# Optimization experiments

Hardware: AMD Instinct MI355X
Metric: run time of the kernel (lower is better)

## Reference

```python
import jax, jax.numpy as jnp
import numpy as np

TEMP = 0.07
EPS = 1e-6
NORM_EPS = 1e-12  # F.normalize default eps
LN_EPS = 1e-5

B, D, H, W = 32, 256, 64, 64
K = 256
DFF = 2048


def _l2norm(v, axis):
    n = jnp.sqrt(jnp.sum(v * v, axis=axis, keepdims=True))
    return v / jnp.maximum(n, NORM_EPS)


def _layernorm(v, g, b):
    mu = jnp.mean(v, axis=-1, keepdims=True)
    var = jnp.mean((v - mu) ** 2, axis=-1, keepdims=True)
    return (v - mu) * jax.lax.rsqrt(var + LN_EPS) * g + b


def setup_inputs() -> dict:
    key = jax.random.key(0)
    ks = jax.random.split(key, 8)
    s1 = 1.0 / np.sqrt(D)
    s2 = 1.0 / np.sqrt(DFF)
    return {
        "x": jax.random.normal(ks[0], (B, D, H, W), jnp.float32),
        "tgt": jax.random.normal(ks[1], (B, K, D), jnp.float32),
        "w1": jax.random.uniform(ks[2], (DFF, D), jnp.float32, -s1, s1),
        "b1": jax.random.uniform(ks[3], (DFF,), jnp.float32, -s1, s1),
        "w2": jax.random.uniform(ks[4], (D, DFF), jnp.float32, -s2, s2),
        "b2": jax.random.uniform(ks[5], (D,), jnp.float32, -s2, s2),
        "g2": jnp.ones((D,), jnp.float32),
        "be2": jnp.zeros((D,), jnp.float32),
        "g3": jnp.ones((D,), jnp.float32),
        "be3": jnp.zeros((D,), jnp.float32),
    }


def reference(x, tgt, w1, b1, w2, b2, g2, be2, g3, be3):
    # slot cross-attention with L2-normalized q/k
    tn = _l2norm(tgt, axis=2)           # (b,k,d)
    xn = _l2norm(x, axis=1)             # (b,d,h,w)
    dots = jnp.einsum('bkd,bdhw->bkhw', tn, xn)
    attn = jax.nn.softmax(dots / TEMP, axis=1) + EPS          # softmax over slots
    attn = attn / jnp.sum(attn, axis=(2, 3), keepdims=True)   # spatial normalization
    tgt2 = jnp.einsum('bdhw,bkhw->bkd', x, attn)
    t = _layernorm(tgt + tgt2, g2, be2)
    # FFN (dropout = identity in eval)
    ff = jnp.maximum(t @ w1.T + b1, 0.0) @ w2.T + b2
    return _layernorm(t + ff, g3, be3)
```

## Files before the change

kernel.cpp:

```cpp
#include <hip/hip_runtime.h>
#include <hip/hip_bf16.h>

using bf16 = __hip_bfloat16;

typedef __attribute__((ext_vector_type(8))) short short8;
typedef __attribute__((ext_vector_type(4))) float f32x4;

constexpr int Bb = 32, Dd = 256, HWw = 4096, Kk = 256, Ff = 2048;
constexpr float TEMP_INV = 1.0f / 0.07f;
constexpr float EPSf = 1e-6f;
constexpr float NORM_EPSf = 1e-12f;
constexpr float LN_EPSf = 1e-5f;

static __device__ __forceinline__ float b2f(bf16 v) { return __bfloat162float(v); }
static __device__ __forceinline__ bf16 f2b(float v) { return __float2bfloat16(v); }


__global__ __launch_bounds__(64) void k_tn(const float* __restrict__ tgt,
                                           bf16* __restrict__ tnbf) {
  int row = blockIdx.x;
  int b = row >> 8, slot = row & 255;
  int lane = threadIdx.x;
  const float* src = tgt + (size_t)row * Dd + lane * 4;
  float v[4];
#pragma unroll
  for (int u = 0; u < 4; u++) v[u] = src[u];
  float ss = v[0] * v[0] + v[1] * v[1] + v[2] * v[2] + v[3] * v[3];
#pragma unroll
  for (int m = 32; m >= 1; m >>= 1) ss += __shfl_xor(ss, m, 64);
  float inv = 1.0f / fmaxf(sqrtf(ss), NORM_EPSf);
  bf16 o[4] __attribute__((aligned(8)));
#pragma unroll
  for (int u = 0; u < 4; u++) o[u] = f2b(v[u] * inv);
  int s = lane >> 3;
  int q2 = (lane >> 1) & 3;
  int jh = (lane & 1) * 4;
  size_t fi = (size_t)((slot >> 4) * 64 + q2 * 16 + (slot & 15));
  *(float2*)(tnbf + ((size_t)(b * 8 + s) * 1024 + fi) * 8 + jh) = *(float2*)o;
}

__global__ __launch_bounds__(64) void k_prew1(const float* __restrict__ w1,
                                              bf16* __restrict__ w1bf) {
  int f = blockIdx.x;
  int lane = threadIdx.x;
  const float* src = w1 + (size_t)f * Dd + lane * 4;
  bf16 o[4] __attribute__((aligned(8)));
#pragma unroll
  for (int u = 0; u < 4; u++) o[u] = f2b(src[u]);
  int s = lane >> 3;
  int q2 = (lane >> 1) & 3;
  int jh = (lane & 1) * 4;
  size_t fi = (size_t)(((f & 63) >> 4) * 64 + q2 * 16 + (f & 15));
  *(float2*)(w1bf + ((size_t)((f >> 6) * 8 + s) * 256 + fi) * 8 + jh) = *(float2*)o;
}

__global__ __launch_bounds__(64) void k_prew2(const float* __restrict__ w2,
                                              bf16* __restrict__ w2bf) {
  int d = blockIdx.x;
  int lane = threadIdx.x;
  const float* src = w2 + (size_t)d * Ff + lane * 32;
  size_t gbase = (size_t)((d >> 6) * 64 + lane) * 256;
  int fbase = ((d & 63) >> 4) * 64 + (d & 15);
#pragma unroll
  for (int q2 = 0; q2 < 4; q2++) {
    float4 v0 = *(const float4*)(src + q2 * 8);
    float4 v1 = *(const float4*)(src + q2 * 8 + 4);
    bf16 o[8] __attribute__((aligned(16)));
    o[0] = f2b(v0.x); o[1] = f2b(v0.y); o[2] = f2b(v0.z); o[3] = f2b(v0.w);
    o[4] = f2b(v1.x); o[5] = f2b(v1.y); o[6] = f2b(v1.z); o[7] = f2b(v1.w);
    *(float4*)(w2bf + (gbase + fbase + q2 * 16) * 8) = *(float4*)o;
  }
}

#define MFMA16(a, b, c) __builtin_amdgcn_mfma_f32_16x16x32_bf16(a, b, c, 0, 0, 0)

__global__ __launch_bounds__(256) void k_dots(const bf16* __restrict__ tnbf,
                                              const float* __restrict__ x,
                                              bf16* __restrict__ xb_bf,
                                              bf16* __restrict__ attn_bf,
                                              float* __restrict__ S) {
  __shared__ __align__(16) char smem[39936];
  bf16* Bs8 = (bf16*)smem;
  float* ssred = (float*)(smem + 33280);
  float* nxl = (float*)(smem + 37632);
  float* red = (float*)(smem + 37888);
  int b = blockIdx.x >> 6;
  int hw0 = (blockIdx.x & 63) * 64;
  int tid = threadIdx.x;
  int wave = tid >> 6, lane = tid & 63;
  int quad = lane >> 4, nl = lane & 15;

  int dp = tid >> 4;
  int ch = tid & 15;
  int qb = dp >> 2;
  int jb = (dp & 3) * 2;

  f32x4 acc[4][4];
#pragma unroll
  for (int i = 0; i < 4; i++)
#pragma unroll
    for (int j = 0; j < 4; j++) acc[i][j] = (f32x4){0.f, 0.f, 0.f, 0.f};
  float ssp[4] = {0.f, 0.f, 0.f, 0.f};

  int spx = (hw0 >> 5) + (ch >> 3);
  int q2x = (ch >> 1) & 3;
  int jx = (ch & 1) * 4;

#pragma unroll 1
  for (int c = 0; c < 2; c++) {
    float4 va4[4], vb4[4];
#pragma unroll
    for (int q = 0; q < 4; q++) {
      const float* xr = x + (size_t)((b << 8) + (c * 4 + q) * 32 + 2 * dp) * HWw + hw0 + ch * 4;
      va4[q] = *(const float4*)xr;
      vb4[q] = *(const float4*)(xr + HWw);
    }
#pragma unroll
    for (int q = 0; q < 4; q++) {
      int s = c * 4 + q;
      float vva[4] = {va4[q].x, va4[q].y, va4[q].z, va4[q].w};
      float vvb[4] = {vb4[q].x, vb4[q].y, vb4[q].z, vb4[q].w};
      bf16 pa[4] __attribute__((aligned(8)));
      bf16 pb[4] __attribute__((aligned(8)));
#pragma unroll
      for (int jj = 0; jj < 4; jj++) {
        ssp[jj] += vva[jj] * vva[jj] + vvb[jj] * vvb[jj];
        pa[jj] = f2b(vva[jj]);
        pb[jj] = f2b(vvb[jj]);
      }
      int d0r = s * 32 + 2 * dp;
      int fiA = (d0r >> 4) * 64 + q2x * 16 + (d0r & 15);
      size_t base = ((size_t)(b * 128) + spx) * 1024;
      *(float2*)(xb_bf + (base + fiA) * 8 + jx) = *(float2*)pa;
      *(float2*)(xb_bf + (base + fiA + 1) * 8 + jx) = *(float2*)pb;
#pragma unroll
      for (int jj = 0; jj < 4; jj++) {
        int hwl = ch * 4 + jj;
        int nt = hwl >> 4;
        int li = (qb << 4) | (hwl & 15);
        union { bf16 h[2]; unsigned int u; } pk;
        pk.h[0] = pa[jj];
        pk.h[1] = pb[jj];
        *(unsigned int*)&Bs8[s * 2080 + nt * 520 + li * 8 + jb] = pk.u;
      }
    }
  }
  __syncthreads();

  short8 afp[4];
  {
    const bf16* ts0 = tnbf + (size_t)(b * 8) * 1024 * 8;
#pragma unroll
    for (int mt = 0; mt < 4; mt++)
      afp[mt] = *(const short8*)(ts0 + (size_t)(((wave << 2) + mt) * 64 + lane) * 8);
  }
  for (int s = 0; s < 8; s++) {
    short8 af[4];
#pragma unroll
    for (int mt = 0; mt < 4; mt++) af[mt] = afp[mt];
    if (s < 7) {
      const bf16* tsrc = tnbf + (size_t)(b * 8 + s + 1) * 1024 * 8;
#pragma unroll
      for (int mt = 0; mt < 4; mt++)
        afp[mt] = *(const short8*)(tsrc + (size_t)(((wave << 2) + mt) * 64 + lane) * 8);
    }
    short8 bfv[4];
#pragma unroll
    for (int nt = 0; nt < 4; nt++)
      bfv[nt] = *(const short8*)(Bs8 + s * 2080 + nt * 520 + lane * 8);
#pragma unroll
    for (int mt = 0; mt < 4; mt++)
#pragma unroll
      for (int nt = 0; nt < 4; nt++) acc[mt][nt] = MFMA16(af[mt], bfv[nt], acc[mt][nt]);
  }

#pragma unroll
  for (int jj = 0; jj < 4; jj++) ssred[(ch * 4 + jj) * 17 + dp] = ssp[jj];
  __syncthreads();
  if (tid < 64) {
    float sum = 0.f;
#pragma unroll
    for (int i = 0; i < 16; i++) sum += ssred[tid * 17 + i];
    nxl[tid] = TEMP_INV / fmaxf(sqrtf(sum), NORM_EPSf);
  }
  __syncthreads();

  float sc[4];
#pragma unroll
  for (int nt = 0; nt < 4; nt++) sc[nt] = nxl[nt * 16 + nl];
#pragma unroll
  for (int mt = 0; mt < 4; mt++)
#pragma unroll
    for (int nt = 0; nt < 4; nt++)
#pragma unroll
      for (int r = 0; r < 4; r++) acc[mt][nt][r] *= sc[nt];

  float* red2 = red + 256;

  float pmax[4];
#pragma unroll
  for (int nt = 0; nt < 4; nt++) {
    float m = acc[0][nt][0];
#pragma unroll
    for (int mt = 0; mt < 4; mt++)
#pragma unroll
      for (int r = 0; r < 4; r++) m = fmaxf(m, acc[mt][nt][r]);
    m = fmaxf(m, __shfl_xor(m, 16, 64));
    m = fmaxf(m, __shfl_xor(m, 32, 64));
    pmax[nt] = m;
  }
  if (lane < 16) {
#pragma unroll
    for (int nt = 0; nt < 4; nt++) red[((wave << 2) + nt) * 16 + nl] = pmax[nt];
  }
  __syncthreads();
  float cmax[4];
#pragma unroll
  for (int nt = 0; nt < 4; nt++) {
    float m = red[nt * 16 + nl];
#pragma unroll
    for (int w2 = 1; w2 < 4; w2++) m = fmaxf(m, red[((w2 << 2) + nt) * 16 + nl]);
    cmax[nt] = m;
  }

  float psum[4];
#pragma unroll
  for (int nt = 0; nt < 4; nt++) {
    float s = 0.f;
#pragma unroll
    for (int mt = 0; mt < 4; mt++)
#pragma unroll
      for (int r = 0; r < 4; r++) {
        float e = __expf(acc[mt][nt][r] - cmax[nt]);
        acc[mt][nt][r] = e;
        s += e;
      }
    s += __shfl_xor(s, 16, 64);
    s += __shfl_xor(s, 32, 64);
    psum[nt] = s;
  }
  if (lane < 16) {
#pragma unroll
    for (int nt = 0; nt < 4; nt++) red2[((wave << 2) + nt) * 16 + nl] = psum[nt];
  }
  __syncthreads();
  float ci[4];
#pragma unroll
  for (int nt = 0; nt < 4; nt++) {
    float s = 0.f;
#pragma unroll
    for (int w2 = 0; w2 < 4; w2++) s += red2[((w2 << 2) + nt) * 16 + nl];
    ci[nt] = 1.0f / s;
  }

#pragma unroll
  for (int mt = 0; mt < 4; mt++) {
    int slotg = (b << 8) + (wave << 6) + (mt << 4) + (quad << 2);
#pragma unroll
    for (int r = 0; r < 4; r++) {
      float rs = 0.f;
#pragma unroll
      for (int nt = 0; nt < 4; nt++) {
        bf16 hb = f2b(acc[mt][nt][r] * ci[nt] + EPSf);
        float q = b2f(hb);
        acc[mt][nt][r] = q;
        rs += q;
      }
      rs += __shfl_xor(rs, 1, 64);
      rs += __shfl_xor(rs, 2, 64);
      rs += __shfl_xor(rs, 4, 64);
      rs += __shfl_xor(rs, 8, 64);
      if (nl == 0) atomicAdd(&S[slotg + r], rs);
    }
  }

  __syncthreads();
  bf16* rp = (bf16*)smem;
  int jat = nl & 7;
#pragma unroll
  for (int h = 0; h < 2; h++) {
#pragma unroll
    for (int mt = 0; mt < 4; mt++) {
      int fi0 = ((wave << 2) + mt) * 64 + (quad << 2);
#pragma unroll
      for (int ntl = 0; ntl < 2; ntl++) {
        int nt = (h << 1) + ntl;
        int q2p = (ntl << 1) + (nl >> 3);
#pragma unroll
        for (int r = 0; r < 4; r++) {
          int fi = fi0 + q2p * 16 + r;
          int fisw = fi ^ ((fi >> 3) & 3);
          rp[fisw * 8 + jat] = f2b(acc[mt][nt][r]);
        }
      }
    }
    __syncthreads();
    size_t gbase = ((size_t)(b * 128) + (hw0 >> 5) + h) * 1024 * 8;
#pragma unroll
    for (int u = 0; u < 4; u++) {
      int fl = u * 256 + tid;
      int fg = fl ^ ((fl >> 3) & 3);
      short8 vv = *(const short8*)(rp + (size_t)fl * 8);
      *(short8*)(attn_bf + gbase + (size_t)fg * 8) = vv;
    }
    if (h == 0) __syncthreads();
  }
}

__global__ __launch_bounds__(256) void k_gemm2(const bf16* __restrict__ attn_bf,
                                               const bf16* __restrict__ xb_bf,
                                               float* __restrict__ t2) {
  int n = blockIdx.x;
  int b = n & 31;
  int r2 = n >> 5;
  int kp = r2 & 3;
  int dgrp = r2 >> 2;
  int tid = threadIdx.x;
  int wave = tid >> 6, lane = tid & 63;
  int wr = wave >> 1, wc = wave & 1;

  f32x4 acc[2][2];
#pragma unroll
  for (int i = 0; i < 2; i++)
#pragma unroll
    for (int j = 0; j < 2; j++) acc[i][j] = (f32x4){0.f, 0.f, 0.f, 0.f};

  const bf16* Abase = attn_bf + ((size_t)(b * 128) * 1024 + (size_t)(kp * 4 + wr * 2) * 64) * 8;
  const bf16* Bbase = xb_bf + ((size_t)(b * 128) * 1024 + (size_t)(dgrp * 4 + wc * 2) * 64) * 8;
#pragma unroll 4
  for (int st = 0; st < 128; st++) {
    const bf16* Ap = Abase + (size_t)st * 1024 * 8;
    const bf16* Bp = Bbase + (size_t)st * 1024 * 8;
    short8 a0 = *(const short8*)(Ap + (size_t)lane * 8);
    short8 a1 = *(const short8*)(Ap + (size_t)(64 + lane) * 8);
    short8 b0 = *(const short8*)(Bp + (size_t)lane * 8);
    short8 b1 = *(const short8*)(Bp + (size_t)(64 + lane) * 8);
    acc[0][0] = MFMA16(a0, b0, acc[0][0]);
    acc[0][1] = MFMA16(a0, b1, acc[0][1]);
    acc[1][0] = MFMA16(a1, b0, acc[1][0]);
    acc[1][1] = MFMA16(a1, b1, acc[1][1]);
  }
  int quad = lane >> 4, nl = lane & 15;
#pragma unroll
  for (int i = 0; i < 2; i++)
#pragma unroll
    for (int r = 0; r < 4; r++) {
      int row = (b << 8) + kp * 64 + wr * 32 + i * 16 + quad * 4 + r;
#pragma unroll
      for (int j = 0; j < 2; j++) {
        int col = dgrp * 64 + wc * 32 + j * 16 + nl;
        t2[(size_t)row * Dd + col] = acc[i][j][r];
      }
    }
}

__global__ __launch_bounds__(64) void k_ln_pre(const float* __restrict__ t2,
                                               const float* __restrict__ S,
                                               const float* __restrict__ tgt,
                                               const float* __restrict__ g,
                                               const float* __restrict__ be,
                                               float* __restrict__ t,
                                               bf16* __restrict__ tbf) {
  int row = blockIdx.x;
  int lane = threadIdx.x;
  float sInv = 1.0f / S[row];
  size_t off = (size_t)row * Dd + lane * 4;
  float4 a0 = *(const float4*)(t2 + off);
  const float* pt = tgt + off;
  float v[4];
  v[0] = a0.x * sInv + pt[0];
  v[1] = a0.y * sInv + pt[1];
  v[2] = a0.z * sInv + pt[2];
  v[3] = a0.w * sInv + pt[3];
  float s1 = v[0] + v[1] + v[2] + v[3];
  float s2 = v[0] * v[0] + v[1] * v[1] + v[2] * v[2] + v[3] * v[3];
#pragma unroll
  for (int m = 32; m >= 1; m >>= 1) {
    s1 += __shfl_xor(s1, m, 64);
    s2 += __shfl_xor(s2, m, 64);
  }
  float mu = s1 * (1.0f / 256.0f);
  float var = s2 * (1.0f / 256.0f) - mu * mu;
  float rs = rsqrtf(fmaxf(var, 0.f) + LN_EPSf);
  float* po = t + (size_t)row * Dd + lane * 4;
  bf16 o[4] __attribute__((aligned(8)));
#pragma unroll
  for (int u = 0; u < 4; u++) {
    float val = (v[u] - mu) * rs * g[lane * 4 + u] + be[lane * 4 + u];
    po[u] = val;
    o[u] = f2b(val);
  }
  int s = lane >> 3;
  int q2 = (lane >> 1) & 3;
  int jh = (lane & 1) * 4;
  size_t fi = (size_t)(((row & 63) >> 4) * 64 + q2 * 16 + (row & 15));
  *(float2*)(tbf + ((size_t)((row >> 6) * 8 + s) * 256 + fi) * 8 + jh) = *(float2*)o;
}

__global__ __launch_bounds__(256) void k_ffn1(const bf16* __restrict__ tbf,
                                              const bf16* __restrict__ w1bf,
                                              const float* __restrict__ b1,
                                              bf16* __restrict__ h1bf) {
  __shared__ __align__(16) bf16 rp[512 * 8];
  int rowgrp = blockIdx.x >> 5;
  int fgrp = blockIdx.x & 31;
  int tid = threadIdx.x;
  int wave = tid >> 6, lane = tid & 63;
  int am = (wave >> 1) * 2, bn = (wave & 1) * 2;

  f32x4 acc[2][2];
#pragma unroll
  for (int i = 0; i < 2; i++)
#pragma unroll
    for (int j = 0; j < 2; j++) acc[i][j] = (f32x4){0.f, 0.f, 0.f, 0.f};

  const bf16* Abase = tbf + (size_t)rowgrp * 8 * 256 * 8;
  const bf16* Bbase = w1bf + (size_t)fgrp * 8 * 256 * 8;
#pragma unroll
  for (int s = 0; s < 8; s++) {
    short8 af[2], bfr[2];
#pragma unroll
    for (int i = 0; i < 2; i++)
      af[i] = *(const short8*)(Abase + ((size_t)s * 256 + ((am + i) * 64 + lane)) * 8);
#pragma unroll
    for (int j = 0; j < 2; j++)
      bfr[j] = *(const short8*)(Bbase + ((size_t)s * 256 + ((bn + j) * 64 + lane)) * 8);
#pragma unroll
    for (int i = 0; i < 2; i++)
#pragma unroll
      for (int j = 0; j < 2; j++) acc[i][j] = MFMA16(af[i], bfr[j], acc[i][j]);
  }
  int quad = lane >> 4, nl = lane & 15;
  int jat = nl & 7;
#pragma unroll
  for (int j = 0; j < 2; j++) {
    int f = fgrp * 64 + (bn + j) * 16 + nl;
    float bias = b1[f];
    int seth = (bn + j) >> 1;
    int q2p = ((bn + j) & 1) * 2 + (nl >> 3);
#pragma unroll
    for (int i = 0; i < 2; i++) {
      int fiBase = (am + i) * 64 + q2p * 16 + (quad << 2);
#pragma unroll
      for (int r = 0; r < 4; r++) {
        float val = fmaxf(acc[i][j][r] + bias, 0.f);
        int fi = fiBase + r;
        int fisw = fi ^ ((fi >> 3) & 3);
        rp[(seth * 256 + fisw) * 8 + jat] = f2b(val);
      }
    }
  }
  __syncthreads();
  size_t sp0 = (size_t)(rowgrp * 64) + fgrp * 2;
#pragma unroll
  for (int u = 0; u < 2; u++) {
    int loc = tid;
    int fg = loc ^ ((loc >> 3) & 3);
    short8 vv = *(const short8*)(rp + ((size_t)u * 256 + loc) * 8);
    *(short8*)(h1bf + ((sp0 + u) * 256 + fg) * 8) = vv;
  }
}

__global__ __launch_bounds__(256) void k_ffn2(const bf16* __restrict__ h1bf,
                                              const bf16* __restrict__ w2bf,
                                              float* __restrict__ o2) {
  __shared__ float redsm[4 * 4160];
  int n = blockIdx.x;
  int rowgrp = n >> 2;
  int cg = n & 3;
  int tid = threadIdx.x;
  int wave = tid >> 6, lane = tid & 63;

  f32x4 acc[4][4];
#pragma unroll
  for (int i = 0; i < 4; i++)
#pragma unroll
    for (int j = 0; j < 4; j++) acc[i][j] = (f32x4){0.f, 0.f, 0.f, 0.f};

#pragma unroll 4
  for (int stl = 0; stl < 16; stl++) {
    int sg = wave * 16 + stl;
    const bf16* Ab = h1bf + ((size_t)(rowgrp * 64 + sg) * 256) * 8;
    const bf16* Bbv = w2bf + ((size_t)(cg * 64 + sg) * 256) * 8;
    short8 af[4], bfr[4];
#pragma unroll
    for (int mt = 0; mt < 4; mt++)
      af[mt] = *(const short8*)(Ab + (size_t)(mt * 64 + lane) * 8);
#pragma unroll
    for (int nt = 0; nt < 4; nt++)
      bfr[nt] = *(const short8*)(Bbv + (size_t)(nt * 64 + lane) * 8);
#pragma unroll
    for (int mt = 0; mt < 4; mt++)
#pragma unroll
      for (int nt = 0; nt < 4; nt++) acc[mt][nt] = MFMA16(af[mt], bfr[nt], acc[mt][nt]);
  }
  int quad = lane >> 4, nl = lane & 15;
  float* my = redsm + wave * 4160;
#pragma unroll
  for (int mt = 0; mt < 4; mt++)
#pragma unroll
    for (int r = 0; r < 4; r++) {
      int row = mt * 16 + quad * 4 + r;
#pragma unroll
      for (int nt = 0; nt < 4; nt++)
        my[row * 65 + nt * 16 + nl] = acc[mt][nt][r];
    }
  __syncthreads();
#pragma unroll
  for (int u = 0; u < 16; u++) {
    int o = u * 256 + tid;
    int row = o >> 6, col = o & 63;
    int li = row * 65 + col;
    float ssum = redsm[li] + redsm[4160 + li] + redsm[8320 + li] + redsm[12480 + li];
    o2[(size_t)(rowgrp * 64 + row) * Dd + cg * 64 + col] = ssum;
  }
}

__global__ __launch_bounds__(64) void k_ln_out(const float* __restrict__ o2,
                                               const float* __restrict__ b2v,
                                               const float* __restrict__ t,
                                               const float* __restrict__ g,
                                               const float* __restrict__ be,
                                               float* __restrict__ out) {
  int row = blockIdx.x;
  int lane = threadIdx.x;
  size_t off = (size_t)row * Dd + lane * 4;
  float4 aq = *(const float4*)(o2 + off);
  const float* pt = t + off;
  float v[4];
  v[0] = aq.x + b2v[lane * 4 + 0] + pt[0];
  v[1] = aq.y + b2v[lane * 4 + 1] + pt[1];
  v[2] = aq.z + b2v[lane * 4 + 2] + pt[2];
  v[3] = aq.w + b2v[lane * 4 + 3] + pt[3];
  float s1 = v[0] + v[1] + v[2] + v[3];
  float s2 = v[0] * v[0] + v[1] * v[1] + v[2] * v[2] + v[3] * v[3];
#pragma unroll
  for (int m = 32; m >= 1; m >>= 1) {
    s1 += __shfl_xor(s1, m, 64);
    s2 += __shfl_xor(s2, m, 64);
  }
  float mu = s1 * (1.0f / 256.0f);
  float var = s2 * (1.0f / 256.0f) - mu * mu;
  float rs = rsqrtf(fmaxf(var, 0.f) + LN_EPSf);
  float* pw = out + (size_t)row * Dd + lane * 4;
#pragma unroll
  for (int u = 0; u < 4; u++)
    pw[u] = (v[u] - mu) * rs * g[lane * 4 + u] + be[lane * 4 + u];
}

extern "C" void kernel_launch(void* const* d_in, const int* in_sizes, int n_in,
                              void* d_out, int out_size, void* d_ws, size_t ws_size,
                              hipStream_t stream) {
  const float* x = (const float*)d_in[0];
  const float* tgt = (const float*)d_in[1];
  const float* w1 = (const float*)d_in[2];
  const float* b1 = (const float*)d_in[3];
  const float* w2 = (const float*)d_in[4];
  const float* b2v = (const float*)d_in[5];
  const float* g2 = (const float*)d_in[6];
  const float* be2 = (const float*)d_in[7];
  const float* g3 = (const float*)d_in[8];
  const float* be3 = (const float*)d_in[9];
  float* out = (float*)d_out;

  char* w = (char*)d_ws;
  bf16* tnbf = (bf16*)w;     w += (size_t)Bb * Kk * Dd * 2;
  float* S = (float*)w;      w += (size_t)Bb * Kk * 4;
  float* t = (float*)w;      w += (size_t)Bb * Kk * Dd * 4;
  bf16* attn_bf = (bf16*)w;  w += (size_t)Bb * HWw * Kk * 2;
  bf16* h1bf = (bf16*)w;     w += (size_t)Bb * Kk * Ff * 2;
  bf16* xb_bf = (bf16*)w;    w += (size_t)Bb * Dd * HWw * 2;

  bf16* tbf = tnbf;
  bf16* w1bf = attn_bf;
  bf16* w2bf = attn_bf + (size_t)Ff * Dd;
  float* t2 = (float*)h1bf;
  float* o2 = (float*)xb_bf;

  hipMemsetAsync(S, 0, (size_t)Bb * Kk * 4, stream);
  k_tn<<<Bb * Kk, 64, 0, stream>>>(tgt, tnbf);
  k_dots<<<Bb * (HWw / 64), 256, 0, stream>>>(tnbf, x, xb_bf, attn_bf, S);
  k_gemm2<<<512, 256, 0, stream>>>(attn_bf, xb_bf, t2);
  k_prew1<<<Ff, 64, 0, stream>>>(w1, w1bf);
  k_prew2<<<Dd, 64, 0, stream>>>(w2, w2bf);
  k_ln_pre<<<Bb * Kk, 64, 0, stream>>>(t2, S, tgt, g2, be2, t, tbf);
  k_ffn1<<<(Bb * Kk / 64) * (Ff / 64), 256, 0, stream>>>(tbf, w1bf, b1, h1bf);
  k_ffn2<<<512, 256, 0, stream>>>(h1bf, w2bf, o2);
  k_ln_out<<<Bb * Kk, 64, 0, stream>>>(o2, b2v, t, g3, be3, out);
}
```

Baseline: 425.6 us.

## Pipeline x loads with MFMA in k_dots using double-buffered LDS chunks

Restructures k_dots so x is loaded in four 2-slice phases into a double-buffered LDS region. The next chunk's global loads are issued while MFMAs run on the current one, and the bf16 xb stores are interleaved with compute. This cuts LDS from about 39KB to 23KB, which may raise occupancy. The cost is four block barriers instead of one, plus more complex scheduling.

```diff
diff --git a/kernel.cpp b/kernel.cpp
--- a/kernel.cpp
+++ b/kernel.cpp
@@ -79,11 +79,11 @@
                                               bf16* __restrict__ xb_bf,
                                               bf16* __restrict__ attn_bf,
                                               float* __restrict__ S) {
-  __shared__ __align__(16) char smem[39936];
-  bf16* Bs8 = (bf16*)smem;
-  float* ssred = (float*)(smem + 33280);
-  float* nxl = (float*)(smem + 37632);
-  float* red = (float*)(smem + 37888);
+  __shared__ __align__(16) char smem[23296];
+  bf16* Bs = (bf16*)smem;
+  float* ssred = (float*)(smem + 16640);
+  float* nxl = (float*)(smem + 20992);
+  float* red = (float*)(smem + 21248);
   int b = blockIdx.x >> 6;
   int hw0 = (blockIdx.x & 63) * 64;
   int tid = threadIdx.x;
@@ -106,72 +106,87 @@
   int q2x = (ch >> 1) & 3;
   int jx = (ch & 1) * 4;
 
+  float4 va4[2], vb4[2];
+#pragma unroll
+  for (int q = 0; q < 2; q++) {
+    const float* xr = x + (size_t)((b << 8) + q * 32 + 2 * dp) * HWw + hw0 + ch * 4;
+    va4[q] = *(const float4*)xr;
+    vb4[q] = *(const float4*)(xr + HWw);
+  }
+  short8 afp[4];
+  {
+    const bf16* ts0 = tnbf + (size_t)(b * 8) * 1024 * 8;
+#pragma unroll
+    for (int mt = 0; mt < 4; mt++)
+      afp[mt] = *(const short8*)(ts0 + (size_t)(((wave << 2) + mt) * 64 + lane) * 8);
+  }
+
 #pragma unroll 1
-  for (int c = 0; c < 2; c++) {
-    float4 va4[4], vb4[4];
-#pragma unroll
-    for (int q = 0; q < 4; q++) {
-      const float* xr = x + (size_t)((b << 8) + (c * 4 + q) * 32 + 2 * dp) * HWw + hw0 + ch * 4;
-      va4[q] = *(const float4*)xr;
-      vb4[q] = *(const float4*)(xr + HWw);
-    }
-#pragma unroll
-    for (int q = 0; q < 4; q++) {
-      int s = c * 4 + q;
+  for (int p = 0; p < 4; p++) {
+    bf16* bsb = Bs + (p & 1) * 2 * 2080;
+    bf16 paS[2][4] __attribute__((aligned(8)));
+    bf16 pbS[2][4] __attribute__((aligned(8)));
+#pragma unroll
+    for (int q = 0; q < 2; q++) {
       float vva[4] = {va4[q].x, va4[q].y, va4[q].z, va4[q].w};
       float vvb[4] = {vb4[q].x, vb4[q].y, vb4[q].z, vb4[q].w};
-      bf16 pa[4] __attribute__((aligned(8)));
-      bf16 pb[4] __attribute__((aligned(8)));
 #pragma unroll
       for (int jj = 0; jj < 4; jj++) {
         ssp[jj] += vva[jj] * vva[jj] + vvb[jj] * vvb[jj];
-        pa[jj] = f2b(vva[jj]);
-        pb[jj] = f2b(vvb[jj]);
-      }
-      int d0r = s * 32 + 2 * dp;
-      int fiA = (d0r >> 4) * 64 + q2x * 16 + (d0r & 15);
-      size_t base = ((size_t)(b * 128) + spx) * 1024;
-      *(float2*)(xb_bf + (base + fiA) * 8 + jx) = *(float2*)pa;
-      *(float2*)(xb_bf + (base + fiA + 1) * 8 + jx) = *(float2*)pb;
+        paS[q][jj] = f2b(vva[jj]);
+        pbS[q][jj] = f2b(vvb[jj]);
+      }
 #pragma unroll
       for (int jj = 0; jj < 4; jj++) {
         int hwl = ch * 4 + jj;
         int nt = hwl >> 4;
         int li = (qb << 4) | (hwl & 15);
         union { bf16 h[2]; unsigned int u; } pk;
-        pk.h[0] = pa[jj];
-        pk.h[1] = pb[jj];
-        *(unsigned int*)&Bs8[s * 2080 + nt * 520 + li * 8 + jb] = pk.u;
-      }
-    }
-  }
-  __syncthreads();
-
-  short8 afp[4];
-  {
-    const bf16* ts0 = tnbf + (size_t)(b * 8) * 1024 * 8;
-#pragma unroll
-    for (int mt = 0; mt < 4; mt++)
-      afp[mt] = *(const short8*)(ts0 + (size_t)(((wave << 2) + mt) * 64 + lane) * 8);
-  }
-  for (int s = 0; s < 8; s++) {
-    short8 af[4];
-#pragma unroll
-    for (int mt = 0; mt < 4; mt++) af[mt] = afp[mt];
-    if (s < 7) {
-      const bf16* tsrc = tnbf + (size_t)(b * 8 + s + 1) * 1024 * 8;
+        pk.h[0] = paS[q][jj];
+        pk.h[1] = pbS[q][jj];
+        *(unsigned int*)&bsb[q * 2080 + nt * 520 + li * 8 + jb] = pk.u;
+      }
+    }
+    __syncthreads();
+
+    if (p < 3) {
+#pragma unroll
+      for (int q = 0; q < 2; q++) {
+        const float* xr = x + (size_t)((b << 8) + ((p + 1) * 2 + q) * 32 + 2 * dp) * HWw + hw0 + ch * 4;
+        va4[q] = *(const float4*)xr;
+        vb4[q] = *(const float4*)(xr + HWw);
+      }
+    }
+#pragma unroll
+    for (int q = 0; q < 2; q++) {
+      int s = 2 * p + q;
+      int d0r = s * 32 + 2 * dp;
+      int fiA = (d0r >> 4) * 64 + q2x * 16 + (d0r & 15);
+      size_t base = ((size_t)(b * 128) + spx) * 1024;
+      *(float2*)(xb_bf + (base + fiA) * 8 + jx) = *(float2*)paS[q];
+      *(float2*)(xb_bf + (base + fiA + 1) * 8 + jx) = *(float2*)pbS[q];
+    }
+#pragma unroll
+    for (int q = 0; q < 2; q++) {
+      int s = 2 * p + q;
+      short8 af[4];
+#pragma unroll
+      for (int mt = 0; mt < 4; mt++) af[mt] = afp[mt];
+      if (s < 7) {
+        const bf16* tsrc = tnbf + (size_t)(b * 8 + s + 1) * 1024 * 8;
+#pragma unroll
+        for (int mt = 0; mt < 4; mt++)
+          afp[mt] = *(const short8*)(tsrc + (size_t)(((wave << 2) + mt) * 64 + lane) * 8);
+      }
+      short8 bfv[4];
+#pragma unroll
+      for (int nt = 0; nt < 4; nt++)
+        bfv[nt] = *(const short8*)(bsb + q * 2080 + nt * 520 + lane * 8);
 #pragma unroll
       for (int mt = 0; mt < 4; mt++)
-        afp[mt] = *(const short8*)(tsrc + (size_t)(((wave << 2) + mt) * 64 + lane) * 8);
-    }
-    short8 bfv[4];
-#pragma unroll
-    for (int nt = 0; nt < 4; nt++)
-      bfv[nt] = *(const short8*)(Bs8 + s * 2080 + nt * 520 + lane * 8);
-#pragma unroll
-    for (int mt = 0; mt < 4; mt++)
-#pragma unroll
-      for (int nt = 0; nt < 4; nt++) acc[mt][nt] = MFMA16(af[mt], bfv[nt], acc[mt][nt]);
+#pragma unroll
+        for (int nt = 0; nt < 4; nt++) acc[mt][nt] = MFMA16(af[mt], bfv[nt], acc[mt][nt]);
+    }
   }
 
 #pragma unroll
```

Result: faster. 391.1 us (-8.1%).

## Overlap x loads with MFMA in k_dots and remap ffn2 blocks per XCD

Applied to the files above, without the earlier changes.

k_dots now splits its staging into two halves. It issues the global loads for the second half of x, then runs the MFMAs on the first half already in LDS, so load latency overlaps with matrix math. The launch bounds now request 3 blocks per SM, which caps register use. k_ffn2 remaps block indices so that the four column-group blocks sharing a row group land on the same XCD, aiming for better L2 reuse of h1bf. The register cap could cause spills, and the extra syncthreads add barrier cost.

```diff
diff --git a/kernel.cpp b/kernel.cpp
--- a/kernel.cpp
+++ b/kernel.cpp
@@ -74,11 +74,11 @@
 
 #define MFMA16(a, b, c) __builtin_amdgcn_mfma_f32_16x16x32_bf16(a, b, c, 0, 0, 0)
 
-__global__ __launch_bounds__(256) void k_dots(const bf16* __restrict__ tnbf,
-                                              const float* __restrict__ x,
-                                              bf16* __restrict__ xb_bf,
-                                              bf16* __restrict__ attn_bf,
-                                              float* __restrict__ S) {
+__global__ __launch_bounds__(256, 3) void k_dots(const bf16* __restrict__ tnbf,
+                                                 const float* __restrict__ x,
+                                                 bf16* __restrict__ xb_bf,
+                                                 bf16* __restrict__ attn_bf,
+                                                 float* __restrict__ S) {
   __shared__ __align__(16) char smem[39936];
   bf16* Bs8 = (bf16*)smem;
   float* ssred = (float*)(smem + 33280);
@@ -106,72 +106,111 @@
   int q2x = (ch >> 1) & 3;
   int jx = (ch & 1) * 4;
 
+  const float* xbase = x + (size_t)((b << 8) + 2 * dp) * HWw + hw0 + ch * 4;
+
+  float4 va4[4], vb4[4];
+  bf16 paS[4][4] __attribute__((aligned(8)));
+  bf16 pbS[4][4] __attribute__((aligned(8)));
+
+#pragma unroll
+  for (int q = 0; q < 4; q++) {
+    const float* xr = xbase + (size_t)(q * 32) * HWw;
+    va4[q] = *(const float4*)xr;
+    vb4[q] = *(const float4*)(xr + HWw);
+  }
+  short8 afp[4];
+  {
+    const bf16* ts0 = tnbf + (size_t)(b * 8) * 1024 * 8;
+#pragma unroll
+    for (int mt = 0; mt < 4; mt++)
+      afp[mt] = *(const short8*)(ts0 + (size_t)(((wave << 2) + mt) * 64 + lane) * 8);
+  }
+#pragma unroll
+  for (int q = 0; q < 4; q++) {
+    float vva[4] = {va4[q].x, va4[q].y, va4[q].z, va4[q].w};
+    float vvb[4] = {vb4[q].x, vb4[q].y, vb4[q].z, vb4[q].w};
+#pragma unroll
+    for (int jj = 0; jj < 4; jj++) {
+      ssp[jj] += vva[jj] * vva[jj] + vvb[jj] * vvb[jj];
+      paS[q][jj] = f2b(vva[jj]);
+      pbS[q][jj] = f2b(vvb[jj]);
+    }
+#pragma unroll
+    for (int jj = 0; jj < 4; jj++) {
+      int hwl = ch * 4 + jj;
+      int nt = hwl >> 4;
+      int li = (qb << 4) | (hwl & 15);
+      union { bf16 h[2]; unsigned int u; } pk;
+      pk.h[0] = paS[q][jj];
+      pk.h[1] = pbS[q][jj];
+      *(unsigned int*)&Bs8[q * 2080 + nt * 520 + li * 8 + jb] = pk.u;
+    }
+  }
+
 #pragma unroll 1
-  for (int c = 0; c < 2; c++) {
-    float4 va4[4], vb4[4];
+  for (int ss = 0; ss < 2; ss++) {
+    __syncthreads();
 #pragma unroll
     for (int q = 0; q < 4; q++) {
-      const float* xr = x + (size_t)((b << 8) + (c * 4 + q) * 32 + 2 * dp) * HWw + hw0 + ch * 4;
-      va4[q] = *(const float4*)xr;
-      vb4[q] = *(const float4*)(xr + HWw);
-    }
-#pragma unroll
-    for (int q = 0; q < 4; q++) {
-      int s = c * 4 + q;
-      float vva[4] = {va4[q].x, va4[q].y, va4[q].z, va4[q].w};
-      float vvb[4] = {vb4[q].x, vb4[q].y, vb4[q].z, vb4[q].w};
-      bf16 pa[4] __attribute__((aligned(8)));
-      bf16 pb[4] __attribute__((aligned(8)));
-#pragma unroll
-      for (int jj = 0; jj < 4; jj++) {
-        ssp[jj] += vva[jj] * vva[jj] + vvb[jj] * vvb[jj];
-        pa[jj] = f2b(vva[jj]);
-        pb[jj] = f2b(vvb[jj]);
-      }
+      int s = 4 * ss + q;
       int d0r = s * 32 + 2 * dp;
       int fiA = (d0r >> 4) * 64 + q2x * 16 + (d0r & 15);
       size_t base = ((size_t)(b * 128) + spx) * 1024;
-      *(float2*)(xb_bf + (base + fiA) * 8 + jx) = *(float2*)pa;
-      *(float2*)(xb_bf + (base + fiA + 1) * 8 + jx) = *(float2*)pb;
-#pragma unroll
-      for (int jj = 0; jj < 4; jj++) {
-        int hwl = ch * 4 + jj;
-        int nt = hwl >> 4;
-        int li = (qb << 4) | (hwl & 15);
-        union { bf16 h[2]; unsigned int u; } pk;
-        pk.h[0] = pa[jj];
-        pk.h[1] = pb[jj];
-        *(unsigned int*)&Bs8[s * 2080 + nt * 520 + li * 8 + jb] = pk.u;
-      }
-    }
-  }
-  __syncthreads();
-
-  short8 afp[4];
-  {
-    const bf16* ts0 = tnbf + (size_t)(b * 8) * 1024 * 8;
-#pragma unroll
-    for (int mt = 0; mt < 4; mt++)
-      afp[mt] = *(const short8*)(ts0 + (size_t)(((wave << 2) + mt) * 64 + lane) * 8);
-  }
-  for (int s = 0; s < 8; s++) {
-    short8 af[4];
-#pragma unroll
-    for (int mt = 0; mt < 4; mt++) af[mt] = afp[mt];
-    if (s < 7) {
-      const bf16* tsrc = tnbf + (size_t)(b * 8 + s + 1) * 1024 * 8;
+      *(float2*)(xb_bf + (base + fiA) * 8 + jx) = *(float2*)paS[q];
+      *(float2*)(xb_bf + (base + fiA + 1) * 8 + jx) = *(float2*)pbS[q];
+    }
+    if (ss == 0) {
+#pragma unroll
+      for (int q = 0; q < 4; q++) {
+        const float* xr = xbase + (size_t)((4 + q) * 32) * HWw;
+        va4[q] = *(const float4*)xr;
+        vb4[q] = *(const float4*)(xr + HWw);
+      }
+    }
+#pragma unroll
+    for (int q = 0; q < 4; q++) {
+      int s = 4 * ss + q;
+      short8 af[4];
+#pragma unroll
+      for (int mt = 0; mt < 4; mt++) af[mt] = afp[mt];
+      if (s < 7) {
+        const bf16* tsrc = tnbf + (size_t)(b * 8 + s + 1) * 1024 * 8;
+#pragma unroll
+        for (int mt = 0; mt < 4; mt++)
+          afp[mt] = *(const short8*)(tsrc + (size_t)(((wave << 2) + mt) * 64 + lane) * 8);
+      }
+      short8 bfv[4];
+#pragma unroll
+      for (int nt = 0; nt < 4; nt++)
+        bfv[nt] = *(const short8*)(Bs8 + (4 * ss + q) * 2080 + nt * 520 + lane * 8);
 #pragma unroll
       for (int mt = 0; mt < 4; mt++)
-        afp[mt] = *(const short8*)(tsrc + (size_t)(((wave << 2) + mt) * 64 + lane) * 8);
-    }
-    short8 bfv[4];
-#pragma unroll
-    for (int nt = 0; nt < 4; nt++)
-      bfv[nt] = *(const short8*)(Bs8 + s * 2080 + nt * 520 + lane * 8);
-#pragma unroll
-    for (int mt = 0; mt < 4; mt++)
-#pragma unroll
-      for (int nt = 0; nt < 4; nt++) acc[mt][nt] = MFMA16(af[mt], bfv[nt], acc[mt][nt]);
+#pragma unroll
+        for (int nt = 0; nt < 4; nt++) acc[mt][nt] = MFMA16(af[mt], bfv[nt], acc[mt][nt]);
+    }
+    if (ss == 0) {
+#pragma unroll
+      for (int q = 0; q < 4; q++) {
+        float vva[4] = {va4[q].x, va4[q].y, va4[q].z, va4[q].w};
+        float vvb[4] = {vb4[q].x, vb4[q].y, vb4[q].z, vb4[q].w};
+#pragma unroll
+        for (int jj = 0; jj < 4; jj++) {
+          ssp[jj] += vva[jj] * vva[jj] + vvb[jj] * vvb[jj];
+          paS[q][jj] = f2b(vva[jj]);
+          pbS[q][jj] = f2b(vvb[jj]);
+        }
+#pragma unroll
+        for (int jj = 0; jj < 4; jj++) {
+          int hwl = ch * 4 + jj;
+          int nt = hwl >> 4;
+          int li = (qb << 4) | (hwl & 15);
+          union { bf16 h[2]; unsigned int u; } pk;
+          pk.h[0] = paS[q][jj];
+          pk.h[1] = pbS[q][jj];
+          *(unsigned int*)&Bs8[(4 + q) * 2080 + nt * 520 + li * 8 + jb] = pk.u;
+        }
+      }
+    }
   }
 
 #pragma unroll
@@ -466,8 +505,10 @@
                                               float* __restrict__ o2) {
   __shared__ float redsm[4 * 4160];
   int n = blockIdx.x;
-  int rowgrp = n >> 2;
-  int cg = n & 3;
+  int xcd = n & 7;
+  int q = n >> 3;
+  int cg = q & 3;
+  int rowgrp = ((q >> 2) << 3) + xcd;
   int tid = threadIdx.x;
   int wave = tid >> 6, lane = tid & 63;
 
```

Result: slower. 456.5 us (+7.3%).
